# Kernel tuning notes

Measured on AMD Instinct MI355X. Metric: run time of the kernel, lower is better.

## Reference

```python
import jax, jax.numpy as jnp
import numpy as np
import math

N = 100000
D = 128      # input_dim
H = 4        # heads
DK = 32      # d_k
DV = D // H  # d_v = 32


def setup_inputs() -> dict:
    key = jax.random.key(0)
    k1, k2, k3, k4, k5 = jax.random.split(key, 5)
    x = jax.random.normal(k1, (N, D), dtype=jnp.float32)
    neighbor_index = jax.random.randint(k2, (N, 4), 0, N, dtype=jnp.int64)
    w_q = jax.random.normal(k3, (H, D, DK), dtype=jnp.float32) * 0.05
    w_k = jax.random.normal(k4, (H, 5, D, DK), dtype=jnp.float32) * 0.05
    w_v = jax.random.normal(k5, (H, 5, D, DV), dtype=jnp.float32) * 0.05
    return {"x": x, "neighbor_index": neighbor_index, "w_q": w_q, "w_k": w_k, "w_v": w_v}


def reference(x, neighbor_index, w_q, w_k, w_v):
    n = x.shape[0]
    d_k = w_q.shape[-1]
    # gather 4 neighbors, prepend self node -> (N, 5, D)
    x_neighbors = jnp.concatenate([x[:, None, :], x[neighbor_index]], axis=1)
    Q = jnp.einsum('nd,hdk->hnk', x, w_q)                 # (H, N, DK)
    K = jnp.einsum('nrd,hrdk->hnrk', x_neighbors, w_k)    # (H, N, 5, DK)
    V = jnp.einsum('nrd,hrdv->hnrv', x_neighbors, w_v)    # (H, N, 5, DV)
    A = jnp.einsum('hnk,hnrk->hnr', Q, K) / math.sqrt(d_k)
    # NOTE: original torch code applies softmax over dim=1, which is the NODE
    # dimension (not the neighbor dimension r). Replicated faithfully.
    A = jax.nn.softmax(A, axis=1)
    Z = jnp.einsum('hnr,hnrv->hnv', A, V)                 # (H, N, DV)
    return Z.transpose(1, 0, 2).reshape(n, -1)            # (N, H*DV)
```

## Files before the change

kernel.cpp:

```cpp
#include <hip/hip_runtime.h>


#define N_NODES 100000
#define D 128
#define H 4
#define R 5
#define NPB 32
#define THREADS 256
#define NBLOCKS (N_NODES / NPB)

typedef _Float16 half_t;
typedef __attribute__((ext_vector_type(2))) _Float16 f16x2;
typedef __attribute__((ext_vector_type(8))) _Float16 f16x8;
typedef __attribute__((ext_vector_type(4))) float f32x4;

typedef const __attribute__((address_space(1))) unsigned int* gp_t;
typedef __attribute__((address_space(3))) unsigned int* lp_t;

__device__ __forceinline__ void async_copy16(const void* g, void* l) {
    __builtin_amdgcn_global_load_lds((gp_t)g, (lp_t)l, 16, 0, 0);
}

__global__ void prep(const float* __restrict__ x,
                     const float* __restrict__ wq, const float* __restrict__ wk,
                     const float* __restrict__ wv,
                     half_t* __restrict__ xh, half_t* __restrict__ wph,
                     float* __restrict__ sums_p)
{
    const int bid = blockIdx.x;
    const int t = threadIdx.x;
    if (bid < 44) {
        const float* src = (bid < 4) ? (wq + bid * 4096)
                         : (bid < 24) ? (wk + (bid - 4) * 4096)
                                      : (wv + (bid - 24) * 4096);
#pragma unroll
        for (int i = 0; i < 16; ++i) {
            int p = t * 16 + i;
            int j = p & 7, ln = (p >> 3) & 63, f = p >> 9;
            int kt = f & 3, mt = f >> 2;
            int d = kt * 32 + (ln >> 4) * 8 + j;
            int ko = mt * 16 + (ln & 15);
            wph[bid * 4096 + p] = (half_t)src[d * 32 + ko];
        }
    } else {
        if (bid == 44) {
            for (int i = t; i < 1280; i += THREADS) sums_p[i] = 0.f;
        }
        const int total = N_NODES * D / 8;
        const int nb = gridDim.x - 44;
        for (int i = (bid - 44) * THREADS + t; i < total; i += nb * THREADS) {
            const float4* s = (const float4*)x + (size_t)i * 2;
            float4 a = s[0], b = s[1];
            f16x8 h8 = {(half_t)a.x, (half_t)a.y, (half_t)a.z, (half_t)a.w,
                        (half_t)b.x, (half_t)b.y, (half_t)b.z, (half_t)b.w};
            *((f16x8*)xh + i) = h8;
        }
    }
}

__device__ __forceinline__ void stage_all(const half_t* __restrict__ xh,
                                          const int* __restrict__ nbr,
                                          int base, char* tile, int tid)
{
    const int w = tid >> 6;
    const int lane = tid & 63;
    const int rr = lane >> 4, c = lane & 15;
    const int rowA = w * 4 + rr;
    const int rowB = rowA + 16;
    const int nodeA = base + rowA;
    const int nodeB = base + rowB;
    int4 a4 = ((const int4*)nbr)[nodeA];
    int4 b4 = ((const int4*)nbr)[nodeB];
    int srcA[5] = {nodeA, a4.x, a4.y, a4.z, a4.w};
    int srcB[5] = {nodeB, b4.x, b4.y, b4.z, b4.w};
    const int sw = ((c ^ (rowA & 7)) << 4);
#pragma unroll
    for (int s = 0; s < 5; ++s) {
        const char* gA = (const char*)xh + (size_t)srcA[s] * 256 + sw;
        const char* gB = (const char*)xh + (size_t)srcB[s] * 256 + sw;
        async_copy16(gA, tile + s * 8192 + (w * 4) * 256);
        async_copy16(gB, tile + s * 8192 + (w * 4 + 16) * 256);
    }
}

__device__ __forceinline__ void load_af(int mid, const half_t* __restrict__ wph,
                                        int lane, f16x8 (&af)[8])
{
#pragma unroll
    for (int kt = 0; kt < 4; ++kt) {
        af[kt * 2]     = *(const f16x8*)(wph + ((mid * 8 + kt) * 64 + lane) * 8);
        af[kt * 2 + 1] = *(const f16x8*)(wph + ((mid * 8 + 4 + kt) * 64 + lane) * 8);
    }
}

__device__ __forceinline__ void proj32(const f16x8 (&af)[8], const half_t* tile,
                                       int lane, f32x4 (&acc)[2][2])
{
    const int l15 = lane & 15, q = lane >> 4;
#pragma unroll
    for (int mt = 0; mt < 2; ++mt)
#pragma unroll
        for (int nt = 0; nt < 2; ++nt)
            acc[mt][nt] = (f32x4){0.f, 0.f, 0.f, 0.f};
#pragma unroll
    for (int kt = 0; kt < 4; ++kt) {
#pragma unroll
        for (int nt = 0; nt < 2; ++nt) {
            int row = nt * 16 + l15;
            int sq = (kt * 4 + q) ^ (row & 7);
            f16x8 b = *(const f16x8*)(tile + row * 128 + sq * 8);
            acc[0][nt] = __builtin_amdgcn_mfma_f32_16x16x32_f16(af[kt * 2], b, acc[0][nt], 0, 0, 0);
            acc[1][nt] = __builtin_amdgcn_mfma_f32_16x16x32_f16(af[kt * 2 + 1], b, acc[1][nt], 0, 0, 0);
        }
    }
}

__global__ __launch_bounds__(THREADS, 4)
void knot_logits(const half_t* __restrict__ xh, const int* __restrict__ nbr,
                 const half_t* __restrict__ wph,
                 half_t* __restrict__ eh, float* __restrict__ sums_p)
{
    __shared__ __align__(16) char smem[5 * 8192];
    const int base = blockIdx.x * NPB;
    const int lane = threadIdx.x & 63;
    const int h = __builtin_amdgcn_readfirstlane((int)(threadIdx.x >> 6));
    const int l15 = lane & 15, q = lane >> 4;

    stage_all(xh, nbr, base, smem, threadIdx.x);

    f16x8 af[8];
    load_af(h, wph, lane, af);
    __syncthreads();

    f32x4 qf[2][2], kf[2][2];
    proj32(af, (const half_t*)smem, lane, qf);

    f16x2 epk[5];
    float esum[5];
#pragma unroll
    for (int r = 0; r < R; ++r) {
        load_af(4 + h * 5 + r, wph, lane, af);
        proj32(af, (const half_t*)(smem + r * 8192), lane, kf);

        float es = 0.f;
#pragma unroll
        for (int nt = 0; nt < 2; ++nt) {
            float p = 0.f;
#pragma unroll
            for (int mt = 0; mt < 2; ++mt)
#pragma unroll
                for (int j = 0; j < 4; ++j)
                    p += qf[mt][nt][j] * kf[mt][nt][j];
            p += __shfl_xor(p, 16, 64);
            p += __shfl_xor(p, 32, 64);
            float e = __expf(p * 0.17677669529663688f);
            epk[r][nt] = (half_t)e;
            es += e;
        }
        es += __shfl_xor(es, 1, 64); es += __shfl_xor(es, 2, 64);
        es += __shfl_xor(es, 4, 64); es += __shfl_xor(es, 8, 64);
        esum[r] = es;
    }

#pragma unroll
    for (int r = 0; r < R; ++r) {
        if (q == 0) {
#pragma unroll
            for (int nt = 0; nt < 2; ++nt)
                eh[(size_t)(h * 5 + r) * N_NODES + base + nt * 16 + l15] = epk[r][nt];
        }
        if (lane == 0)
            atomicAdd(&sums_p[(h * 5 + r) * 64 + (blockIdx.x & 63)], esum[r]);
    }
}

#define ZS 132
__global__ __launch_bounds__(THREADS, 4)
void knot_out(const half_t* __restrict__ xh, const int* __restrict__ nbr,
              const half_t* __restrict__ wph, const half_t* __restrict__ eh,
              const float* __restrict__ sums_p, float* __restrict__ out)
{
    __shared__ __align__(16) char smem[5 * 8192];
    const int base = blockIdx.x * NPB;
    const int lane = threadIdx.x & 63;
    const int h = __builtin_amdgcn_readfirstlane((int)(threadIdx.x >> 6));
    const int l15 = lane & 15, q = lane >> 4;

    stage_all(xh, nbr, base, smem, threadIdx.x);

    float inv[5];
#pragma unroll
    for (int r = 0; r < R; ++r) {
        float v = sums_p[(h * 5 + r) * 64 + lane];
        v += __shfl_xor(v, 1, 64);  v += __shfl_xor(v, 2, 64);
        v += __shfl_xor(v, 4, 64);  v += __shfl_xor(v, 8, 64);
        v += __shfl_xor(v, 16, 64); v += __shfl_xor(v, 32, 64);
        inv[r] = 1.0f / v;
    }
    float ev[5][2];
#pragma unroll
    for (int r = 0; r < R; ++r)
#pragma unroll
        for (int nt = 0; nt < 2; ++nt)
            ev[r][nt] = (float)eh[(size_t)(h * 5 + r) * N_NODES + base + nt * 16 + l15];

    f16x8 af[8];
    load_af(24 + h * 5 + 0, wph, lane, af);
    __syncthreads();

    f32x4 z[2][2], vf[2][2];
#pragma unroll
    for (int mt = 0; mt < 2; ++mt)
#pragma unroll
        for (int nt = 0; nt < 2; ++nt)
            z[mt][nt] = (f32x4){0.f, 0.f, 0.f, 0.f};

#pragma unroll
    for (int r = 0; r < R; ++r) {
        proj32(af, (const half_t*)(smem + r * 8192), lane, vf);
        if (r < R - 1) load_af(24 + h * 5 + r + 1, wph, lane, af);
#pragma unroll
        for (int nt = 0; nt < 2; ++nt) {
            float w = ev[r][nt] * inv[r];
#pragma unroll
            for (int mt = 0; mt < 2; ++mt)
#pragma unroll
                for (int j = 0; j < 4; ++j)
                    z[mt][nt][j] += w * vf[mt][nt][j];
        }
    }

    __syncthreads();
    float* zt = (float*)smem;
#pragma unroll
    for (int mt = 0; mt < 2; ++mt)
#pragma unroll
        for (int nt = 0; nt < 2; ++nt) {
            int node = nt * 16 + l15;
            int col = h * 32 + mt * 16 + q * 4;
            *(f32x4*)(zt + node * ZS + col) = z[mt][nt];
        }
    __syncthreads();
    {
        const int row = threadIdx.x >> 3;
        const int c = threadIdx.x & 7;
        float* dst = out + (size_t)(base + row) * D + c * 16;
        const float* srcp = zt + row * ZS + c * 16;
#pragma unroll
        for (int i4 = 0; i4 < 4; ++i4)
            *(float4*)(dst + i4 * 4) = *(const float4*)(srcp + i4 * 4);
    }
}

extern "C" void kernel_launch(void* const* d_in, const int* in_sizes, int n_in,
                              void* d_out, int out_size, void* d_ws, size_t ws_size,
                              hipStream_t stream)
{
    const float* x   = (const float*)d_in[0];
    const int*   nbr = (const int*)d_in[1];
    const float* w_q = (const float*)d_in[2];
    const float* w_k = (const float*)d_in[3];
    const float* w_v = (const float*)d_in[4];
    float* out = (float*)d_out;

    float*  sums_p = (float*)d_ws;
    half_t* eh     = (half_t*)((char*)d_ws + 8192);
    half_t* wph    = (half_t*)((char*)d_ws + 4194304);
    half_t* xh     = (half_t*)((char*)d_ws + 4718592);

    prep<<<44 + 2048, THREADS, 0, stream>>>(x, w_q, w_k, w_v, xh, wph, sums_p);
    knot_logits<<<NBLOCKS, THREADS, 0, stream>>>(xh, nbr, wph, eh, sums_p);
    knot_out<<<NBLOCKS, THREADS, 0, stream>>>(xh, nbr, wph, eh, sums_p, out);
}
```

Measured before the change: 184.6 us.

## Materialize exp-weighted V in workspace and stream-normalize instead of recomputing projections

Adds a fused kernel that computes Q, K, the exponentiated logits and V in one pass, then writes exp-weighted V values in fp16 to a large workspace buffer along with the per-head/neighbor exp sums. A lightweight streaming kernel then reduces the sums, normalizes and accumulates the five neighbor contributions per output. This avoids re-gathering neighbors and redoing the K/V projection in a second pass, at the cost of writing and reading about 128 MB of intermediate data. The new path runs only when the workspace is large enough; otherwise it falls back to the old two-kernel path.

```diff
diff --git a/kernel.cpp b/kernel.cpp
--- a/kernel.cpp
+++ b/kernel.cpp
@@ -11,6 +11,7 @@
 
 typedef _Float16 half_t;
 typedef __attribute__((ext_vector_type(2))) _Float16 f16x2;
+typedef __attribute__((ext_vector_type(4))) _Float16 f16x4;
 typedef __attribute__((ext_vector_type(8))) _Float16 f16x8;
 typedef __attribute__((ext_vector_type(4))) float f32x4;
 
@@ -116,6 +117,113 @@
 }
 
 __global__ __launch_bounds__(THREADS, 4)
+void knot_qkv(const half_t* __restrict__ xh, const int* __restrict__ nbr,
+              const half_t* __restrict__ wph,
+              half_t* __restrict__ Yg, float* __restrict__ sums_p)
+{
+    __shared__ __align__(16) char smem[5 * 8192];
+    const int base = blockIdx.x * NPB;
+    const int lane = threadIdx.x & 63;
+    const int h = __builtin_amdgcn_readfirstlane((int)(threadIdx.x >> 6));
+    const int l15 = lane & 15, q = lane >> 4;
+
+    stage_all(xh, nbr, base, smem, threadIdx.x);
+
+    f16x8 af[8];
+    load_af(h, wph, lane, af);
+    __syncthreads();
+
+    f32x4 qf[2][2], kf[2][2];
+    proj32(af, (const half_t*)smem, lane, qf);
+
+    float esum[5];
+#pragma unroll
+    for (int r = 0; r < R; ++r) {
+        load_af(4 + h * 5 + r, wph, lane, af);
+        proj32(af, (const half_t*)(smem + r * 8192), lane, kf);
+
+        float er[2];
+        float es = 0.f;
+#pragma unroll
+        for (int nt = 0; nt < 2; ++nt) {
+            float p = 0.f;
+#pragma unroll
+            for (int mt = 0; mt < 2; ++mt)
+#pragma unroll
+                for (int j = 0; j < 4; ++j)
+                    p += qf[mt][nt][j] * kf[mt][nt][j];
+            p += __shfl_xor(p, 16, 64);
+            p += __shfl_xor(p, 32, 64);
+            float e = __expf(p * 0.17677669529663688f);
+            er[nt] = e;
+            es += e;
+        }
+        es += __shfl_xor(es, 1, 64); es += __shfl_xor(es, 2, 64);
+        es += __shfl_xor(es, 4, 64); es += __shfl_xor(es, 8, 64);
+        esum[r] = es;
+
+        load_af(24 + h * 5 + r, wph, lane, af);
+        proj32(af, (const half_t*)(smem + r * 8192), lane, kf);
+        half_t* yr = Yg + ((size_t)(h * 5 + r) * N_NODES + base) * 32;
+#pragma unroll
+        for (int nt = 0; nt < 2; ++nt) {
+            float w = er[nt];
+#pragma unroll
+            for (int mt = 0; mt < 2; ++mt) {
+                f16x4 y4 = {(half_t)(kf[mt][nt][0] * w), (half_t)(kf[mt][nt][1] * w),
+                            (half_t)(kf[mt][nt][2] * w), (half_t)(kf[mt][nt][3] * w)};
+                *(f16x4*)(yr + (nt * 16 + l15) * 32 + mt * 16 + q * 4) = y4;
+            }
+        }
+    }
+
+#pragma unroll
+    for (int r = 0; r < R; ++r)
+        if (lane == 0)
+            atomicAdd(&sums_p[(h * 5 + r) * 64 + (blockIdx.x & 63)], esum[r]);
+}
+
+__global__ __launch_bounds__(256, 8)
+void knot_stream(const half_t* __restrict__ Yg, const float* __restrict__ sums_p,
+                 float* __restrict__ out)
+{
+    const int lane = threadIdx.x & 63;
+    const int h = __builtin_amdgcn_readfirstlane((int)(threadIdx.x >> 6));
+    const int n16 = lane >> 2, k = lane & 3;
+
+    float inv[5];
+#pragma unroll
+    for (int r = 0; r < R; ++r) {
+        float v = sums_p[(h * 5 + r) * 64 + lane];
+        v += __shfl_xor(v, 1, 64);  v += __shfl_xor(v, 2, 64);
+        v += __shfl_xor(v, 4, 64);  v += __shfl_xor(v, 8, 64);
+        v += __shfl_xor(v, 16, 64); v += __shfl_xor(v, 32, 64);
+        inv[r] = 1.0f / v;
+    }
+
+    const int base = blockIdx.x * 64;
+#pragma unroll
+    for (int i = 0; i < 4; ++i) {
+        const int node = base + i * 16 + n16;
+        if (node < N_NODES) {
+            float z[8];
+#pragma unroll
+            for (int j = 0; j < 8; ++j) z[j] = 0.f;
+#pragma unroll
+            for (int r = 0; r < R; ++r) {
+                f16x8 y = *(const f16x8*)(Yg + ((size_t)(h * 5 + r) * N_NODES + node) * 32 + k * 8);
+#pragma unroll
+                for (int j = 0; j < 8; ++j)
+                    z[j] += inv[r] * (float)y[j];
+            }
+            float* dst = out + (size_t)node * D + h * 32 + k * 8;
+            *(f32x4*)dst       = (f32x4){z[0], z[1], z[2], z[3]};
+            *(f32x4*)(dst + 4) = (f32x4){z[4], z[5], z[6], z[7]};
+        }
+    }
+}
+
+__global__ __launch_bounds__(THREADS, 4)
 void knot_logits(const half_t* __restrict__ xh, const int* __restrict__ nbr,
                  const half_t* __restrict__ wph,
                  half_t* __restrict__ eh, float* __restrict__ sums_p)
@@ -267,8 +375,15 @@
     half_t* eh     = (half_t*)((char*)d_ws + 8192);
     half_t* wph    = (half_t*)((char*)d_ws + 4194304);
     half_t* xh     = (half_t*)((char*)d_ws + 4718592);
+    half_t* Yg     = (half_t*)((char*)d_ws + 33554432ull);
+    const size_t need = 33554432ull + 128000000ull;
 
     prep<<<44 + 2048, THREADS, 0, stream>>>(x, w_q, w_k, w_v, xh, wph, sums_p);
-    knot_logits<<<NBLOCKS, THREADS, 0, stream>>>(xh, nbr, wph, eh, sums_p);
-    knot_out<<<NBLOCKS, THREADS, 0, stream>>>(xh, nbr, wph, eh, sums_p, out);
-}
+    if (ws_size >= need) {
+        knot_qkv<<<NBLOCKS, THREADS, 0, stream>>>(xh, nbr, wph, Yg, sums_p);
+        knot_stream<<<(N_NODES + 63) / 64, 256, 0, stream>>>(Yg, sums_p, out);
+    } else {
+        knot_logits<<<NBLOCKS, THREADS, 0, stream>>>(xh, nbr, wph, eh, sums_p);
+        knot_out<<<NBLOCKS, THREADS, 0, stream>>>(xh, nbr, wph, eh, sums_p, out);
+    }
+}
```

Result: slower. 211.6 us (+14.7%).

## Compute softmax sums from fp8 copy of x and recompute logits in output kernel

Applied to the files above, without the earlier changes.

Prep now also writes an fp8 (e4m3) copy of x. A new sums kernel gathers the fp8 rows, which halves the gather bytes, and computes only the per-column exp sums, processing two node groups per block. The output kernel recomputes Q·K logits in fp16 instead of reading stored exp values, so the eh buffer and its writes and reads go away. The cost is extra Q/K projection MFMA work in the final kernel. There is also an accuracy risk: the normalizer comes from fp8 logits while the numerators come from fp16 logits, so they no longer match exactly.

```diff
diff --git a/kernel.cpp b/kernel.cpp
--- a/kernel.cpp
+++ b/kernel.cpp
@@ -10,22 +10,69 @@
 #define NBLOCKS (N_NODES / NPB)
 
 typedef _Float16 half_t;
-typedef __attribute__((ext_vector_type(2))) _Float16 f16x2;
 typedef __attribute__((ext_vector_type(8))) _Float16 f16x8;
 typedef __attribute__((ext_vector_type(4))) float f32x4;
+typedef __attribute__((ext_vector_type(2))) float f32x2;
 
 typedef const __attribute__((address_space(1))) unsigned int* gp_t;
 typedef __attribute__((address_space(3))) unsigned int* lp_t;
 
 __device__ __forceinline__ void async_copy16(const void* g, void* l) {
     __builtin_amdgcn_global_load_lds((gp_t)g, (lp_t)l, 16, 0, 0);
+}
+
+__device__ __forceinline__ unsigned enc1(float f) {
+    float a = fabsf(f);
+    a = fminf(a, 448.f);
+    unsigned s = f < 0.f ? 0x80u : 0u;
+    if (a < 0.015625f) {
+        unsigned m = (unsigned)(int)rintf(a * 512.f);
+        return s | m;
+    }
+    int E = (int)((__float_as_uint(a) >> 23) & 255) - 127;
+    float sc = __uint_as_float((unsigned)(3 - E + 127) << 23);
+    int m = (int)rintf(a * sc);
+    if (m == 16) { m = 8; ++E; }
+    return s | (unsigned)((E + 7) << 3) | (unsigned)(m - 8);
+}
+
+__device__ __forceinline__ unsigned enc_pk4(float a, float b, float c, float d) {
+#if __has_builtin(__builtin_amdgcn_cvt_pk_fp8_f32)
+    unsigned w = (unsigned)__builtin_amdgcn_cvt_pk_fp8_f32(a, b, 0, false);
+    w = (unsigned)__builtin_amdgcn_cvt_pk_fp8_f32(c, d, (int)w, true);
+    return w;
+#else
+    return enc1(a) | (enc1(b) << 8) | (enc1(c) << 16) | (enc1(d) << 24);
+#endif
+}
+
+__device__ __forceinline__ f16x8 dec8(uint2 v) {
+#if __has_builtin(__builtin_amdgcn_cvt_pk_f32_fp8)
+    f32x2 p0 = __builtin_amdgcn_cvt_pk_f32_fp8(v.x, false);
+    f32x2 p1 = __builtin_amdgcn_cvt_pk_f32_fp8(v.x, true);
+    f32x2 p2 = __builtin_amdgcn_cvt_pk_f32_fp8(v.y, false);
+    f32x2 p3 = __builtin_amdgcn_cvt_pk_f32_fp8(v.y, true);
+    return (f16x8){(half_t)p0.x, (half_t)p0.y, (half_t)p1.x, (half_t)p1.y,
+                   (half_t)p2.x, (half_t)p2.y, (half_t)p3.x, (half_t)p3.y};
+#else
+    f16x8 r;
+#pragma unroll
+    for (int i = 0; i < 8; ++i) {
+        unsigned b = ((i < 4) ? (v.x >> (8 * i)) : (v.y >> (8 * (i - 4)))) & 0xffu;
+        unsigned e = (b >> 3) & 15u, m = b & 7u;
+        float mag = (e == 0) ? (float)m * 0.001953125f
+                             : __uint_as_float(((e + 120u) << 23) | (m << 20));
+        r[i] = (half_t)((b & 0x80u) ? -mag : mag);
+    }
+    return r;
+#endif
 }
 
 __global__ void prep(const float* __restrict__ x,
                      const float* __restrict__ wq, const float* __restrict__ wk,
                      const float* __restrict__ wv,
-                     half_t* __restrict__ xh, half_t* __restrict__ wph,
-                     float* __restrict__ sums_p)
+                     half_t* __restrict__ xh, unsigned char* __restrict__ xq,
+                     half_t* __restrict__ wph, float* __restrict__ sums_p)
 {
     const int bid = blockIdx.x;
     const int t = threadIdx.x;
@@ -54,6 +101,10 @@
             f16x8 h8 = {(half_t)a.x, (half_t)a.y, (half_t)a.z, (half_t)a.w,
                         (half_t)b.x, (half_t)b.y, (half_t)b.z, (half_t)b.w};
             *((f16x8*)xh + i) = h8;
+            uint2 t8;
+            t8.x = enc_pk4(a.x, a.y, a.z, a.w);
+            t8.y = enc_pk4(b.x, b.y, b.z, b.w);
+            ((uint2*)xq)[i] = t8;
         }
     }
 }
@@ -83,6 +134,26 @@
     }
 }
 
+__device__ __forceinline__ void stage_all8(const unsigned char* __restrict__ xq,
+                                           const int* __restrict__ nbr,
+                                           int base, char* tile, int tid)
+{
+    const int w = tid >> 6;
+    const int lane = tid & 63;
+    const int ro = lane >> 3;
+    const int c = lane & 7;
+    const int row = w * 8 + ro;
+    const int node = base + row;
+    int4 a4 = ((const int4*)nbr)[node];
+    int src[5] = {node, a4.x, a4.y, a4.z, a4.w};
+    const int sw = ((c ^ (row & 7)) << 4);
+#pragma unroll
+    for (int s = 0; s < 5; ++s) {
+        const char* g = (const char*)xq + (size_t)src[s] * 128 + sw;
+        async_copy16(g, tile + s * 4096 + (w * 8) * 128);
+    }
+}
+
 __device__ __forceinline__ void load_af(int mid, const half_t* __restrict__ wph,
                                         int lane, f16x8 (&af)[8])
 {
@@ -115,33 +186,45 @@
     }
 }
 
-__global__ __launch_bounds__(THREADS, 4)
-void knot_logits(const half_t* __restrict__ xh, const int* __restrict__ nbr,
-                 const half_t* __restrict__ wph,
-                 half_t* __restrict__ eh, float* __restrict__ sums_p)
-{
-    __shared__ __align__(16) char smem[5 * 8192];
-    const int base = blockIdx.x * NPB;
-    const int lane = threadIdx.x & 63;
-    const int h = __builtin_amdgcn_readfirstlane((int)(threadIdx.x >> 6));
+__device__ __forceinline__ void proj32q(const f16x8 (&af)[8], const char* tile,
+                                        int lane, f32x4 (&acc)[2][2])
+{
     const int l15 = lane & 15, q = lane >> 4;
-
-    stage_all(xh, nbr, base, smem, threadIdx.x);
-
+#pragma unroll
+    for (int mt = 0; mt < 2; ++mt)
+#pragma unroll
+        for (int nt = 0; nt < 2; ++nt)
+            acc[mt][nt] = (f32x4){0.f, 0.f, 0.f, 0.f};
+#pragma unroll
+    for (int kt = 0; kt < 4; ++kt) {
+#pragma unroll
+        for (int nt = 0; nt < 2; ++nt) {
+            int row = nt * 16 + l15;
+            int kc = kt * 2 + (q >> 1);
+            uint2 v = *(const uint2*)(tile + row * 128 +
+                                      ((kc ^ (row & 7)) << 4) + (q & 1) * 8);
+            f16x8 b = dec8(v);
+            acc[0][nt] = __builtin_amdgcn_mfma_f32_16x16x32_f16(af[kt * 2], b, acc[0][nt], 0, 0, 0);
+            acc[1][nt] = __builtin_amdgcn_mfma_f32_16x16x32_f16(af[kt * 2 + 1], b, acc[1][nt], 0, 0, 0);
+        }
+    }
+}
+
+__device__ __forceinline__ void sums_group(const char* tile, int bidx,
+                                           const half_t* __restrict__ wph,
+                                           float* __restrict__ sums_p,
+                                           int lane, int h)
+{
     f16x8 af[8];
     load_af(h, wph, lane, af);
-    __syncthreads();
-
     f32x4 qf[2][2], kf[2][2];
-    proj32(af, (const half_t*)smem, lane, qf);
-
-    f16x2 epk[5];
+    proj32q(af, tile, lane, qf);
+
     float esum[5];
 #pragma unroll
     for (int r = 0; r < R; ++r) {
         load_af(4 + h * 5 + r, wph, lane, af);
-        proj32(af, (const half_t*)(smem + r * 8192), lane, kf);
-
+        proj32q(af, tile + r * 4096, lane, kf);
         float es = 0.f;
 #pragma unroll
         for (int nt = 0; nt < 2; ++nt) {
@@ -153,32 +236,42 @@
                     p += qf[mt][nt][j] * kf[mt][nt][j];
             p += __shfl_xor(p, 16, 64);
             p += __shfl_xor(p, 32, 64);
-            float e = __expf(p * 0.17677669529663688f);
-            epk[r][nt] = (half_t)e;
-            es += e;
+            es += __expf(p * 0.17677669529663688f);
         }
         es += __shfl_xor(es, 1, 64); es += __shfl_xor(es, 2, 64);
         es += __shfl_xor(es, 4, 64); es += __shfl_xor(es, 8, 64);
         esum[r] = es;
     }
-
-#pragma unroll
-    for (int r = 0; r < R; ++r) {
-        if (q == 0) {
-#pragma unroll
-            for (int nt = 0; nt < 2; ++nt)
-                eh[(size_t)(h * 5 + r) * N_NODES + base + nt * 16 + l15] = epk[r][nt];
-        }
+#pragma unroll
+    for (int r = 0; r < R; ++r)
         if (lane == 0)
-            atomicAdd(&sums_p[(h * 5 + r) * 64 + (blockIdx.x & 63)], esum[r]);
-    }
+            atomicAdd(&sums_p[(h * 5 + r) * 64 + (bidx & 63)], esum[r]);
+}
+
+__global__ __launch_bounds__(THREADS, 4)
+void knot_sums(const unsigned char* __restrict__ xq, const int* __restrict__ nbr,
+               const half_t* __restrict__ wph, float* __restrict__ sums_p)
+{
+    __shared__ __align__(16) char smem[2 * 5 * 4096];
+    const int g0 = blockIdx.x * 64;
+    const int g1 = g0 + 32;
+    const int lane = threadIdx.x & 63;
+    const int h = __builtin_amdgcn_readfirstlane((int)(threadIdx.x >> 6));
+    const bool has2 = (g1 < N_NODES);
+
+    stage_all8(xq, nbr, g0, smem, threadIdx.x);
+    if (has2) stage_all8(xq, nbr, g1, smem + 20480, threadIdx.x);
+    __syncthreads();
+
+    sums_group(smem, blockIdx.x, wph, sums_p, lane, h);
+    if (has2) sums_group(smem + 20480, blockIdx.x, wph, sums_p, lane, h);
 }
 
 #define ZS 132
 __global__ __launch_bounds__(THREADS, 4)
-void knot_out(const half_t* __restrict__ xh, const int* __restrict__ nbr,
-              const half_t* __restrict__ wph, const half_t* __restrict__ eh,
-              const float* __restrict__ sums_p, float* __restrict__ out)
+void knot_all(const half_t* __restrict__ xh, const int* __restrict__ nbr,
+              const half_t* __restrict__ wph, const float* __restrict__ sums_p,
+              float* __restrict__ out)
 {
     __shared__ __align__(16) char smem[5 * 8192];
     const int base = blockIdx.x * NPB;
@@ -197,18 +290,13 @@
         v += __shfl_xor(v, 16, 64); v += __shfl_xor(v, 32, 64);
         inv[r] = 1.0f / v;
     }
-    float ev[5][2];
-#pragma unroll
-    for (int r = 0; r < R; ++r)
-#pragma unroll
-        for (int nt = 0; nt < 2; ++nt)
-            ev[r][nt] = (float)eh[(size_t)(h * 5 + r) * N_NODES + base + nt * 16 + l15];
 
     f16x8 af[8];
-    load_af(24 + h * 5 + 0, wph, lane, af);
+    load_af(h, wph, lane, af);
     __syncthreads();
 
-    f32x4 z[2][2], vf[2][2];
+    f32x4 qf[2][2], t[2][2], z[2][2];
+    proj32(af, (const half_t*)smem, lane, qf);
 #pragma unroll
     for (int mt = 0; mt < 2; ++mt)
 #pragma unroll
@@ -217,16 +305,31 @@
 
 #pragma unroll
     for (int r = 0; r < R; ++r) {
-        proj32(af, (const half_t*)(smem + r * 8192), lane, vf);
-        if (r < R - 1) load_af(24 + h * 5 + r + 1, wph, lane, af);
-#pragma unroll
-        for (int nt = 0; nt < 2; ++nt) {
-            float w = ev[r][nt] * inv[r];
+        load_af(4 + h * 5 + r, wph, lane, af);
+        proj32(af, (const half_t*)(smem + r * 8192), lane, t);
+        float er[2];
+#pragma unroll
+        for (int nt = 0; nt < 2; ++nt) {
+            float p = 0.f;
 #pragma unroll
             for (int mt = 0; mt < 2; ++mt)
 #pragma unroll
                 for (int j = 0; j < 4; ++j)
-                    z[mt][nt][j] += w * vf[mt][nt][j];
+                    p += qf[mt][nt][j] * t[mt][nt][j];
+            p += __shfl_xor(p, 16, 64);
+            p += __shfl_xor(p, 32, 64);
+            er[nt] = __expf(p * 0.17677669529663688f);
+        }
+        load_af(24 + h * 5 + r, wph, lane, af);
+        proj32(af, (const half_t*)(smem + r * 8192), lane, t);
+#pragma unroll
+        for (int nt = 0; nt < 2; ++nt) {
+            float w = er[nt] * inv[r];
+#pragma unroll
+            for (int mt = 0; mt < 2; ++mt)
+#pragma unroll
+                for (int j = 0; j < 4; ++j)
+                    z[mt][nt][j] += w * t[mt][nt][j];
         }
     }
 
@@ -263,12 +366,12 @@
     const float* w_v = (const float*)d_in[4];
     float* out = (float*)d_out;
 
-    float*  sums_p = (float*)d_ws;
-    half_t* eh     = (half_t*)((char*)d_ws + 8192);
-    half_t* wph    = (half_t*)((char*)d_ws + 4194304);
-    half_t* xh     = (half_t*)((char*)d_ws + 4718592);
-
-    prep<<<44 + 2048, THREADS, 0, stream>>>(x, w_q, w_k, w_v, xh, wph, sums_p);
-    knot_logits<<<NBLOCKS, THREADS, 0, stream>>>(xh, nbr, wph, eh, sums_p);
-    knot_out<<<NBLOCKS, THREADS, 0, stream>>>(xh, nbr, wph, eh, sums_p, out);
-}
+    float*         sums_p = (float*)d_ws;
+    half_t*        wph    = (half_t*)((char*)d_ws + 4194304);
+    half_t*        xh     = (half_t*)((char*)d_ws + 4718592);
+    unsigned char* xq     = (unsigned char*)d_ws + 30408704;
+
+    prep<<<44 + 2048, THREADS, 0, stream>>>(x, w_q, w_k, w_v, xh, xq, wph, sums_p);
+    knot_sums<<<(N_NODES + 63) / 64, THREADS, 0, stream>>>(xq, nbr, wph, sums_p);
+    knot_all<<<NBLOCKS, THREADS, 0, stream>>>(xh, nbr, wph, sums_p, out);
+}
```

New measurement: 302.7 us. 64.0% more time.
